# Kernel tuning notes

Hardware: AMD Instinct MI355X
Metric: run time of the kernel (lower is better)

The kernel has to match this reference:

```python
import jax, jax.numpy as jnp
import numpy as np

N = 100000   # batched tree nodes
WD = 300     # word_dim
TD = 50      # tag_dim
M = 168      # mem_dim


def setup_inputs() -> dict:
    key = jax.random.key(0)
    ks = jax.random.split(key, 17)
    rn = lambda k, shp: jax.random.normal(k, shp, dtype=jnp.float32)
    w = lambda k, shp: jax.random.normal(k, shp, dtype=jnp.float32) * 0.05
    return {
        "e": rn(ks[0], (N, WD)),
        "tag": rn(ks[1], (N, TD)),
        "tag_parent": rn(ks[2], (N, TD)),
        "h_prev": rn(ks[3], (N, M)),
        "c_prev": rn(ks[4], (N, M)),
        "k": rn(ks[5], (N, M)),
        "q": rn(ks[6], (N, M)),
        # Leaf cell: 4 gates (i, o, f_left, u), each with We/Wt/Wtp/Uh linears,
        # fused as stacked [in_dim, 4*M] matrices + one fused bias.
        "We_l": w(ks[7], (WD, 4 * M)),
        "Wt_l": w(ks[8], (TD, 4 * M)),
        "Wtp_l": w(ks[9], (TD, 4 * M)),
        "Uh_l": w(ks[10], (M, 4 * M)),
        "b_l": w(ks[11], (4 * M,)),
        # Node cell: 5 gates (i, o, f_left, f_down, u) with Wt/Wtp/Uh; the Uk
        # (child-sum k) linear is only applied to the first 4 gates (u omits it,
        # per the source).
        "Wt_n": w(ks[12], (TD, 5 * M)),
        "Wtp_n": w(ks[13], (TD, 5 * M)),
        "Uh_n": w(ks[14], (M, 5 * M)),
        "Uk_n": w(ks[15], (M, 4 * M)),
        "b_n": w(ks[16], (5 * M,)),
    }


def reference(e, tag, tag_parent, h_prev, c_prev, k, q,
              We_l, Wt_l, Wtp_l, Uh_l, b_l,
              Wt_n, Wtp_n, Uh_n, Uk_n, b_n):
    sig, tanh = jax.nn.sigmoid, jnp.tanh
    # ---- LeafModule ----
    pre = e @ We_l + tag @ Wt_l + tag_parent @ Wtp_l + h_prev @ Uh_l + b_l  # [N, 4M]
    i, o, fl, u = jnp.split(pre, 4, axis=-1)
    c1 = sig(i) * tanh(u) + sig(fl) * c_prev
    h1 = sig(o) * tanh(c1)
    # ---- NodeModule (consumes leaf state as h_prev / c_prev) ----
    pre5 = tag @ Wt_n + tag_parent @ Wtp_n + h1 @ Uh_n + b_n  # [N, 5M]
    pre4 = k @ Uk_n                                            # [N, 4M]
    i2, o2, fl2, fd2, u2 = jnp.split(pre5, 5, axis=-1)
    ki, ko, kfl, kfd = jnp.split(pre4, 4, axis=-1)
    i2, o2, fl2, fd2 = i2 + ki, o2 + ko, fl2 + kfl, fd2 + kfd
    c2 = sig(i2) * tanh(u2) + sig(fd2) * q + sig(fl2) * c1
    h2 = sig(o2) * tanh(c2)
    return jnp.concatenate([h2, c2], axis=-1)  # [N, 2M]
```

## Files before the change

### kernel.cpp

```cpp
#include <hip/hip_runtime.h>
#include <hip/hip_bf16.h>

#define NROWS 100000

typedef __attribute__((ext_vector_type(8))) short bf16x8;
typedef __attribute__((ext_vector_type(4))) float f32x4;
typedef float f32x4a8 __attribute__((ext_vector_type(4), aligned(8)));

__device__ __forceinline__ short f2b(float f) {
  __hip_bfloat16 h = __float2bfloat16(f);
  short s;
  __builtin_memcpy(&s, &h, sizeof(s));
  return s;
}

__device__ __forceinline__ float b2f(unsigned short u) {
  unsigned v = ((unsigned)u) << 16;
  float f;
  __builtin_memcpy(&f, &v, sizeof(f));
  return f;
}

__device__ __forceinline__ float sigf(float x) { return 1.f / (1.f + __expf(-x)); }
__device__ __forceinline__ float tanh_f(float x) { return 1.f - 2.f / (__expf(2.f * x) + 1.f); }

__device__ __forceinline__ void gload_lds16(const void* g, void* l) {
  __builtin_amdgcn_global_load_lds((const __attribute__((address_space(1))) unsigned int*)g,
                                   (__attribute__((address_space(3))) unsigned int*)l, 16, 0, 0);
}

__global__ void pack_weights(const float* __restrict__ We_l, const float* __restrict__ Wt_l,
                             const float* __restrict__ Wtp_l, const float* __restrict__ Uh_l,
                             const float* __restrict__ b_l,
                             const float* __restrict__ Wt_n, const float* __restrict__ Wtp_n,
                             const float* __restrict__ Uh_n, const float* __restrict__ Uk_n,
                             const float* __restrict__ b_n,
                             unsigned short* __restrict__ B1, unsigned short* __restrict__ B2) {
  const int NB1 = 18 * 3 * 16 * 512;
  const int NB2 = 14 * 3 * 24 * 512;
  int idx = blockIdx.x * blockDim.x + threadIdx.x;
  if (idx < NB1) {
    int b = idx & 7, lane = (idx >> 3) & 63, t = idx >> 9;
    int ct = t % 16, mb = (t / 16) % 3, kt = t / 48;
    int k = kt * 32 + ((lane >> 4) << 3) + b;
    int gate = ct >> 2, mtl = ct & 3;
    int m = mb * 64 + mtl * 16 + (lane & 15);
    float v = 0.f;
    if (m < 168) {
      int col = gate * 168 + m;
      if (k < 300)       v = We_l[k * 672 + col];
      else if (k < 350)  v = Wt_l[(k - 300) * 672 + col];
      else if (k < 400)  v = Wtp_l[(k - 350) * 672 + col];
      else if (k < 568)  v = Uh_l[(k - 400) * 672 + col];
      else if (k == 568) v = b_l[col];
    }
    B1[idx] = (unsigned short)f2b(v);
  } else if (idx < NB1 + NB2) {
    int j = idx - NB1;
    int b = j & 7, lane = (j >> 3) & 63, t = j >> 9;
    int ct = t % 24, mb = (t / 24) % 3, kt = t / 72;
    int k = kt * 32 + ((lane >> 4) << 3) + b;
    int gate = ct >> 2, mtl = ct & 3;
    int m = mb * 64 + mtl * 16 + (lane & 15);
    float v = 0.f;
    if (ct < 20 && m < 168) {
      int col = gate * 168 + m;
      if (k < 50)        v = Wt_n[k * 840 + col];
      else if (k < 100)  v = Wtp_n[(k - 50) * 840 + col];
      else if (k < 268)  v = (gate < 4) ? Uk_n[(k - 100) * 672 + gate * 168 + m] : 0.f;
      else if (k < 436)  v = Uh_n[(k - 268) * 840 + col];
      else if (k == 436) v = b_n[col];
    }
    B2[j] = (unsigned short)f2b(v);
  }
}

__device__ __forceinline__ float4 ld4a8(const float* __restrict__ p) {
  f32x4a8 v = *(const f32x4a8*)p;
  return make_float4(v[0], v[1], v[2], v[3]);
}

#define G1_NKT 18
#define G1_LOADS 2

__global__ __launch_bounds__(512, 4) void gemm1_kernel(
    const float* __restrict__ e, const float* __restrict__ tg, const float* __restrict__ tp,
    const float* __restrict__ hp, const float* __restrict__ cprev,
    const char* __restrict__ B1, unsigned short* __restrict__ c1buf,
    unsigned short* __restrict__ h1buf) {
  __shared__ char bb[2][16 * 1024];
  __shared__ char ab[2][4096];
  const int tid = threadIdx.x;
  const int wave = tid >> 6, ln = tid & 63;
  const int rw = wave >> 2, cw = wave & 3;
  const int rowblk = blockIdx.x / 3, mb = blockIdx.x % 3;
  const int rbase = rowblk * 64 + rw * 32;
  const int c = ln & 15, rg = ln >> 4;

  const int srowt = tid >> 3;
  const int sks = tid & 7;
  int srow = rowblk * 64 + srowt;
  if (srow >= NROWS) srow = NROWS - 1;
  const int sphys = srowt * 64 + ((((sks >> 1) ^ ((srowt >> 1) & 3)) << 4)) + ((sks & 1) << 3);

  auto loadA = [&](int kt) -> float4 {
    const int c4 = kt * 32 + sks * 4;
    if (c4 + 4 <= 300) return *(const float4*)(e + srow * 300 + c4);
    if (c4 >= 300 && c4 + 4 <= 348) return ld4a8(tg + srow * 50 + (c4 - 300));
    if (c4 == 348)
      return make_float4(tg[srow * 50 + 48], tg[srow * 50 + 49], tp[srow * 50 + 0], tp[srow * 50 + 1]);
    if (c4 >= 352 && c4 + 4 <= 400) return ld4a8(tp + srow * 50 + (c4 - 350));
    if (c4 >= 400 && c4 + 4 <= 568) return *(const float4*)(hp + srow * 168 + (c4 - 400));
    if (c4 == 568) return make_float4(1.f, 0.f, 0.f, 0.f);
    return make_float4(0.f, 0.f, 0.f, 0.f);
  };
  auto storeA = [&](int buf, float4 v) {
    ushort4 w;
    w.x = (unsigned short)f2b(v.x); w.y = (unsigned short)f2b(v.y);
    w.z = (unsigned short)f2b(v.z); w.w = (unsigned short)f2b(v.w);
    *(ushort4*)&ab[buf][sphys] = w;
  };

  f32x4 acc[2][4];
  const f32x4 z4 = {0.f, 0.f, 0.f, 0.f};
#pragma unroll
  for (int a = 0; a < 2; ++a)
#pragma unroll
    for (int t = 0; t < 4; ++t) acc[a][t] = z4;

  storeA(0, loadA(0));
  const char* Bbase = B1 + (size_t)mb * 16384;
#pragma unroll
  for (int j = 0; j < G1_LOADS; ++j)
    gload_lds16(Bbase + (j * 512 + tid) * 16, &bb[0][(j * 512 + (wave << 6)) * 16]);
  float4 av = loadA(1);
  __syncthreads();

  const int r0t = rw * 32 + c, r1t = rw * 32 + 16 + c;
  const int aoff0 = r0t * 64 + ((rg ^ ((r0t >> 1) & 3)) << 4);
  const int aoff1 = r1t * 64 + ((rg ^ ((r1t >> 1) & 3)) << 4);

#pragma unroll
  for (int kt = 0; kt < G1_NKT; ++kt) {
    const int cur = kt & 1, nxt = cur ^ 1;
    bf16x8 a0 = *(const bf16x8*)&ab[cur][aoff0];
    bf16x8 a1 = *(const bf16x8*)&ab[cur][aoff1];
    bf16x8 bfr[4];
#pragma unroll
    for (int g = 0; g < 4; ++g)
      bfr[g] = *(const bf16x8*)&bb[cur][((((g << 2) + cw) << 6) + ln) * 16];
    if (kt + 1 < G1_NKT) {
      storeA(nxt, av);
      if (kt + 2 < G1_NKT) av = loadA(kt + 2);
      const char* g = B1 + ((size_t)(kt + 1) * 3 + mb) * 16384;
#pragma unroll
      for (int j = 0; j < G1_LOADS; ++j)
        gload_lds16(g + (j * 512 + tid) * 16, &bb[nxt][(j * 512 + (wave << 6)) * 16]);
    }
#pragma unroll
    for (int g = 0; g < 4; ++g) {
      acc[0][g] = __builtin_amdgcn_mfma_f32_16x16x32_bf16(a0, bfr[g], acc[0][g], 0, 0, 0);
      acc[1][g] = __builtin_amdgcn_mfma_f32_16x16x32_bf16(a1, bfr[g], acc[1][g], 0, 0, 0);
    }
    __syncthreads();
  }

  const int m = mb * 64 + cw * 16 + c;
  if (m < 168) {
#pragma unroll
    for (int rt = 0; rt < 2; ++rt) {
#pragma unroll
      for (int reg = 0; reg < 4; ++reg) {
        const int row = rbase + rt * 16 + (rg << 2) + reg;
        if (row >= NROWS) continue;
        const float iv = acc[rt][0][reg];
        const float ov = acc[rt][1][reg];
        const float fv = acc[rt][2][reg];
        const float uv = acc[rt][3][reg];
        const int off = row * 168 + m;
        const float cp = cprev[off];
        const float c1 = sigf(iv) * tanh_f(uv) + sigf(fv) * cp;
        const float h1 = sigf(ov) * tanh_f(c1);
        c1buf[off] = (unsigned short)f2b(c1);
        h1buf[off] = (unsigned short)f2b(h1);
      }
    }
  }
}

#define G2_NKT 14
#define G2_LOADS 3

__global__ __launch_bounds__(512, 4) void gemm2_kernel(
    const float* __restrict__ tg, const float* __restrict__ tp, const float* __restrict__ kk,
    const float* __restrict__ q, const char* __restrict__ B2,
    const unsigned short* __restrict__ c1buf, const unsigned short* __restrict__ h1buf,
    float* __restrict__ out) {
  __shared__ char bb[2][24 * 1024];
  __shared__ char ab[2][4096];
  const int tid = threadIdx.x;
  const int wave = tid >> 6, ln = tid & 63;
  const int rw = wave >> 2, cw = wave & 3;
  const int rowblk = blockIdx.x / 3, mb = blockIdx.x % 3;
  const int rbase = rowblk * 64 + rw * 32;
  const int c = ln & 15, rg = ln >> 4;

  const int srowt = tid >> 3;
  const int sks = tid & 7;
  int srow = rowblk * 64 + srowt;
  if (srow >= NROWS) srow = NROWS - 1;
  const int sphys = srowt * 64 + ((((sks >> 1) ^ ((srowt >> 1) & 3)) << 4)) + ((sks & 1) << 3);

  auto loadA = [&](int kt) -> float4 {
    const int c4 = kt * 32 + sks * 4;
    if (c4 + 4 <= 48) return ld4a8(tg + srow * 50 + c4);
    if (c4 == 48)
      return make_float4(tg[srow * 50 + 48], tg[srow * 50 + 49], tp[srow * 50 + 0], tp[srow * 50 + 1]);
    if (c4 >= 52 && c4 + 4 <= 100) return ld4a8(tp + srow * 50 + (c4 - 50));
    if (c4 >= 100 && c4 + 4 <= 268) return *(const float4*)(kk + srow * 168 + (c4 - 100));
    if (c4 >= 268 && c4 + 4 <= 436) {
      ushort4 w = *(const ushort4*)(h1buf + srow * 168 + (c4 - 268));
      return make_float4(b2f(w.x), b2f(w.y), b2f(w.z), b2f(w.w));
    }
    if (c4 == 436) return make_float4(1.f, 0.f, 0.f, 0.f);
    return make_float4(0.f, 0.f, 0.f, 0.f);
  };
  auto storeA = [&](int buf, float4 v) {
    ushort4 w;
    w.x = (unsigned short)f2b(v.x); w.y = (unsigned short)f2b(v.y);
    w.z = (unsigned short)f2b(v.z); w.w = (unsigned short)f2b(v.w);
    *(ushort4*)&ab[buf][sphys] = w;
  };

  f32x4 acc[2][5];
  const f32x4 z4 = {0.f, 0.f, 0.f, 0.f};
#pragma unroll
  for (int a = 0; a < 2; ++a)
#pragma unroll
    for (int t = 0; t < 5; ++t) acc[a][t] = z4;

  storeA(0, loadA(0));
  const char* Bbase = B2 + (size_t)mb * 24576;
#pragma unroll
  for (int j = 0; j < G2_LOADS; ++j)
    gload_lds16(Bbase + (j * 512 + tid) * 16, &bb[0][(j * 512 + (wave << 6)) * 16]);
  float4 av = loadA(1);
  __syncthreads();

  const int r0t = rw * 32 + c, r1t = rw * 32 + 16 + c;
  const int aoff0 = r0t * 64 + ((rg ^ ((r0t >> 1) & 3)) << 4);
  const int aoff1 = r1t * 64 + ((rg ^ ((r1t >> 1) & 3)) << 4);

#pragma unroll
  for (int kt = 0; kt < G2_NKT; ++kt) {
    const int cur = kt & 1, nxt = cur ^ 1;
    bf16x8 a0 = *(const bf16x8*)&ab[cur][aoff0];
    bf16x8 a1 = *(const bf16x8*)&ab[cur][aoff1];
    bf16x8 bfr[5];
#pragma unroll
    for (int g = 0; g < 5; ++g)
      bfr[g] = *(const bf16x8*)&bb[cur][((((g << 2) + cw) << 6) + ln) * 16];
    if (kt + 1 < G2_NKT) {
      storeA(nxt, av);
      if (kt + 2 < G2_NKT) av = loadA(kt + 2);
      const char* g = B2 + ((size_t)(kt + 1) * 3 + mb) * 24576;
#pragma unroll
      for (int j = 0; j < G2_LOADS; ++j)
        gload_lds16(g + (j * 512 + tid) * 16, &bb[nxt][(j * 512 + (wave << 6)) * 16]);
    }
#pragma unroll
    for (int g = 0; g < 5; ++g) {
      acc[0][g] = __builtin_amdgcn_mfma_f32_16x16x32_bf16(a0, bfr[g], acc[0][g], 0, 0, 0);
      acc[1][g] = __builtin_amdgcn_mfma_f32_16x16x32_bf16(a1, bfr[g], acc[1][g], 0, 0, 0);
    }
    __syncthreads();
  }

  const int m = mb * 64 + cw * 16 + c;
  if (m < 168) {
#pragma unroll
    for (int rt = 0; rt < 2; ++rt) {
#pragma unroll
      for (int reg = 0; reg < 4; ++reg) {
        const int row = rbase + rt * 16 + (rg << 2) + reg;
        if (row >= NROWS) continue;
        const float i2 = acc[rt][0][reg];
        const float o2 = acc[rt][1][reg];
        const float fl2 = acc[rt][2][reg];
        const float fd2 = acc[rt][3][reg];
        const float u2 = acc[rt][4][reg];
        const int off = row * 168 + m;
        const float c1 = b2f(c1buf[off]);
        const float qv = q[off];
        const float c2 = sigf(i2) * tanh_f(u2) + sigf(fd2) * qv + sigf(fl2) * c1;
        const float h2 = sigf(o2) * tanh_f(c2);
        out[row * 336 + m] = h2;
        out[row * 336 + 168 + m] = c2;
      }
    }
  }
}

extern "C" void kernel_launch(void* const* d_in, const int* in_sizes, int n_in,
                              void* d_out, int out_size, void* d_ws, size_t ws_size,
                              hipStream_t stream) {
  const float* e     = (const float*)d_in[0];
  const float* tag   = (const float*)d_in[1];
  const float* tagp  = (const float*)d_in[2];
  const float* hprev = (const float*)d_in[3];
  const float* cprev = (const float*)d_in[4];
  const float* kk    = (const float*)d_in[5];
  const float* q     = (const float*)d_in[6];
  const float* We_l  = (const float*)d_in[7];
  const float* Wt_l  = (const float*)d_in[8];
  const float* Wtp_l = (const float*)d_in[9];
  const float* Uh_l  = (const float*)d_in[10];
  const float* b_l   = (const float*)d_in[11];
  const float* Wt_n  = (const float*)d_in[12];
  const float* Wtp_n = (const float*)d_in[13];
  const float* Uh_n  = (const float*)d_in[14];
  const float* Uk_n  = (const float*)d_in[15];
  const float* b_n   = (const float*)d_in[16];
  float* out = (float*)d_out;

  char* ws = (char*)d_ws;
  unsigned short* B1 = (unsigned short*)ws;
  unsigned short* B2 = (unsigned short*)(ws + (1 << 20));
  unsigned short* c1buf = (unsigned short*)(ws + (3 << 20));
  unsigned short* h1buf = (unsigned short*)(ws + (3 << 20) + 33600000);

  const int NB = 18 * 3 * 16 * 512 + 14 * 3 * 24 * 512;
  pack_weights<<<(NB + 255) / 256, 256, 0, stream>>>(We_l, Wt_l, Wtp_l, Uh_l, b_l,
                                                     Wt_n, Wtp_n, Uh_n, Uk_n, b_n, B1, B2);

  const int nblk = ((NROWS + 63) / 64) * 3;
  gemm1_kernel<<<nblk, 512, 0, stream>>>(e, tag, tagp, hprev, cprev,
                                         (const char*)B1, c1buf, h1buf);
  gemm2_kernel<<<nblk, 512, 0, stream>>>(tag, tagp, kk, q,
                                         (const char*)B2, c1buf, h1buf, out);
}
```

Before: 489.7 us.

## Replace LDS-staged GEMMs with per-wave register tiles loading operands directly

Both GEMM kernels drop shared-memory staging and barriers. Each wave now owns a 64-row (gemm1) or 48-row (gemm2) by 16-column tile covering all gates. A and B fragments are loaded straight from global memory into registers with double-buffered prefetch. The weight packing is reordered per column tile, and the node cell's K order puts h1 first so its bf16 data can be fed to MFMA without conversion. This removes LDS traffic and __syncthreads, but gives up cross-wave reuse of A and B through LDS, so global and L2 loads rise and register pressure grows.

```diff
diff --git a/kernel.cpp b/kernel.cpp
--- a/kernel.cpp
+++ b/kernel.cpp
@@ -2,6 +2,10 @@
 #include <hip/hip_bf16.h>
 
 #define NROWS 100000
+#define G1_NRB 1563
+#define G2_NRB 2084
+#define G1_NT (G1_NRB * 11)
+#define G2_NT (G2_NRB * 11)
 
 typedef __attribute__((ext_vector_type(8))) short bf16x8;
 typedef __attribute__((ext_vector_type(4))) float f32x4;
@@ -14,20 +18,35 @@
   return s;
 }
 
-__device__ __forceinline__ float b2f(unsigned short u) {
-  unsigned v = ((unsigned)u) << 16;
-  float f;
-  __builtin_memcpy(&f, &v, sizeof(f));
-  return f;
-}
-
 __device__ __forceinline__ float sigf(float x) { return 1.f / (1.f + __expf(-x)); }
 __device__ __forceinline__ float tanh_f(float x) { return 1.f - 2.f / (__expf(2.f * x) + 1.f); }
 
-__device__ __forceinline__ void gload_lds16(const void* g, void* l) {
-  __builtin_amdgcn_global_load_lds((const __attribute__((address_space(1))) unsigned int*)g,
-                                   (__attribute__((address_space(3))) unsigned int*)l, 16, 0, 0);
-}
+__device__ __forceinline__ float4 ld4a8(const float* __restrict__ p) {
+  f32x4a8 v = *(const f32x4a8*)p;
+  return make_float4(v[0], v[1], v[2], v[3]);
+}
+
+__device__ __forceinline__ float4 u2f4(uint4 u) {
+  float4 f;
+  __builtin_memcpy(&f, &u, 16);
+  return f;
+}
+
+__device__ __forceinline__ bf16x8 raw2bf8(float4 lo) {
+  bf16x8 r;
+  __builtin_memcpy(&r, &lo, 16);
+  return r;
+}
+
+__device__ __forceinline__ bf16x8 cvt2bf8(float4 lo, float4 hi) {
+  bf16x8 r;
+  r[0] = f2b(lo.x); r[1] = f2b(lo.y); r[2] = f2b(lo.z); r[3] = f2b(lo.w);
+  r[4] = f2b(hi.x); r[5] = f2b(hi.y); r[6] = f2b(hi.z); r[7] = f2b(hi.w);
+  return r;
+}
+
+#define NB1R (18 * 11 * 4 * 512)
+#define NB2R (14 * 11 * 5 * 512)
 
 __global__ void pack_weights(const float* __restrict__ We_l, const float* __restrict__ Wt_l,
                              const float* __restrict__ Wtp_l, const float* __restrict__ Uh_l,
@@ -35,16 +54,14 @@
                              const float* __restrict__ Wt_n, const float* __restrict__ Wtp_n,
                              const float* __restrict__ Uh_n, const float* __restrict__ Uk_n,
                              const float* __restrict__ b_n,
-                             unsigned short* __restrict__ B1, unsigned short* __restrict__ B2) {
-  const int NB1 = 18 * 3 * 16 * 512;
-  const int NB2 = 14 * 3 * 24 * 512;
+                             unsigned short* __restrict__ B1r, unsigned short* __restrict__ B2r) {
   int idx = blockIdx.x * blockDim.x + threadIdx.x;
-  if (idx < NB1) {
-    int b = idx & 7, lane = (idx >> 3) & 63, t = idx >> 9;
-    int ct = t % 16, mb = (t / 16) % 3, kt = t / 48;
+  if (idx < NB1R) {
+    int b = idx & 7, lane = (idx >> 3) & 63, fr = idx >> 9;
+    int gate = fr & 3, tmp = fr >> 2;
+    int mt = tmp % 11, kt = tmp / 11;
     int k = kt * 32 + ((lane >> 4) << 3) + b;
-    int gate = ct >> 2, mtl = ct & 3;
-    int m = mb * 64 + mtl * 16 + (lane & 15);
+    int m = mt * 16 + (lane & 15);
     float v = 0.f;
     if (m < 168) {
       int col = gate * 168 + m;
@@ -54,130 +71,122 @@
       else if (k < 568)  v = Uh_l[(k - 400) * 672 + col];
       else if (k == 568) v = b_l[col];
     }
-    B1[idx] = (unsigned short)f2b(v);
-  } else if (idx < NB1 + NB2) {
-    int j = idx - NB1;
-    int b = j & 7, lane = (j >> 3) & 63, t = j >> 9;
-    int ct = t % 24, mb = (t / 24) % 3, kt = t / 72;
+    B1r[idx] = (unsigned short)f2b(v);
+  } else if (idx < NB1R + NB2R) {
+    int j = idx - NB1R;
+    int b = j & 7, lane = (j >> 3) & 63, fr = j >> 9;
+    int gate = fr % 5, tmp = fr / 5;
+    int mt = tmp % 11, kt = tmp / 11;
     int k = kt * 32 + ((lane >> 4) << 3) + b;
-    int gate = ct >> 2, mtl = ct & 3;
-    int m = mb * 64 + mtl * 16 + (lane & 15);
+    int m = mt * 16 + (lane & 15);
     float v = 0.f;
-    if (ct < 20 && m < 168) {
+    if (m < 168) {
       int col = gate * 168 + m;
-      if (k < 50)        v = Wt_n[k * 840 + col];
-      else if (k < 100)  v = Wtp_n[(k - 50) * 840 + col];
-      else if (k < 268)  v = (gate < 4) ? Uk_n[(k - 100) * 672 + gate * 168 + m] : 0.f;
-      else if (k < 436)  v = Uh_n[(k - 268) * 840 + col];
+      if (k < 168)       v = Uh_n[k * 840 + col];
+      else if (k < 218)  v = Wt_n[(k - 168) * 840 + col];
+      else if (k < 268)  v = Wtp_n[(k - 218) * 840 + col];
+      else if (k < 436)  v = (gate < 4) ? Uk_n[(k - 268) * 672 + gate * 168 + m] : 0.f;
       else if (k == 436) v = b_n[col];
     }
-    B2[j] = (unsigned short)f2b(v);
-  }
-}
-
-__device__ __forceinline__ float4 ld4a8(const float* __restrict__ p) {
-  f32x4a8 v = *(const f32x4a8*)p;
-  return make_float4(v[0], v[1], v[2], v[3]);
-}
-
-#define G1_NKT 18
-#define G1_LOADS 2
-
-__global__ __launch_bounds__(512, 4) void gemm1_kernel(
+    B2r[j] = (unsigned short)f2b(v);
+  }
+}
+
+__global__ __launch_bounds__(256, 3) void gemm1_kernel(
     const float* __restrict__ e, const float* __restrict__ tg, const float* __restrict__ tp,
     const float* __restrict__ hp, const float* __restrict__ cprev,
-    const char* __restrict__ B1, unsigned short* __restrict__ c1buf,
+    const unsigned short* __restrict__ B1r, unsigned short* __restrict__ c1buf,
     unsigned short* __restrict__ h1buf) {
-  __shared__ char bb[2][16 * 1024];
-  __shared__ char ab[2][4096];
-  const int tid = threadIdx.x;
-  const int wave = tid >> 6, ln = tid & 63;
-  const int rw = wave >> 2, cw = wave & 3;
-  const int rowblk = blockIdx.x / 3, mb = blockIdx.x % 3;
-  const int rbase = rowblk * 64 + rw * 32;
+  const int tid = threadIdx.x, wave = tid >> 6, ln = tid & 63;
+  const int wid = blockIdx.x * 4 + wave;
+  if (wid >= G1_NT) return;
+  const int rb = wid / 11, mt = wid - rb * 11;
   const int c = ln & 15, rg = ln >> 4;
-
-  const int srowt = tid >> 3;
-  const int sks = tid & 7;
-  int srow = rowblk * 64 + srowt;
-  if (srow >= NROWS) srow = NROWS - 1;
-  const int sphys = srowt * 64 + ((((sks >> 1) ^ ((srowt >> 1) & 3)) << 4)) + ((sks & 1) << 3);
-
-  auto loadA = [&](int kt) -> float4 {
-    const int c4 = kt * 32 + sks * 4;
-    if (c4 + 4 <= 300) return *(const float4*)(e + srow * 300 + c4);
-    if (c4 >= 300 && c4 + 4 <= 348) return ld4a8(tg + srow * 50 + (c4 - 300));
-    if (c4 == 348)
-      return make_float4(tg[srow * 50 + 48], tg[srow * 50 + 49], tp[srow * 50 + 0], tp[srow * 50 + 1]);
-    if (c4 >= 352 && c4 + 4 <= 400) return ld4a8(tp + srow * 50 + (c4 - 350));
-    if (c4 >= 400 && c4 + 4 <= 568) return *(const float4*)(hp + srow * 168 + (c4 - 400));
-    if (c4 == 568) return make_float4(1.f, 0.f, 0.f, 0.f);
-    return make_float4(0.f, 0.f, 0.f, 0.f);
+  const int k0base = rg << 3;
+
+  int row[4];
+#pragma unroll
+  for (int rt = 0; rt < 4; ++rt) {
+    int r = rb * 64 + rt * 16 + c;
+    row[rt] = r < NROWS ? r : NROWS - 1;
+  }
+  const char* bptr = (const char*)B1r + (size_t)mt * 4096 + (size_t)ln * 16;
+
+  auto loadA = [&](int kt, int rt, float4& lo, float4& hi) {
+    const int k0 = kt * 32 + k0base;
+    const int r = row[rt];
+    if (k0 + 8 <= 300) {
+      const float* p = e + r * 300 + k0;
+      lo = *(const float4*)p; hi = *(const float4*)(p + 4);
+    } else if (k0 == 296) {
+      lo = *(const float4*)(e + r * 300 + 296);
+      hi = ld4a8(tg + r * 50);
+    } else if (k0 >= 304 && k0 + 8 <= 350) {
+      const float* p = tg + r * 50 + (k0 - 300);
+      lo = ld4a8(p); hi = ld4a8(p + 4);
+    } else if (k0 == 344) {
+      lo = ld4a8(tg + r * 50 + 44);
+      hi = make_float4(tg[r * 50 + 48], tg[r * 50 + 49], tp[r * 50 + 0], tp[r * 50 + 1]);
+    } else if (k0 >= 352 && k0 + 8 <= 400) {
+      const float* p = tp + r * 50 + (k0 - 350);
+      lo = ld4a8(p); hi = ld4a8(p + 4);
+    } else if (k0 >= 400 && k0 + 8 <= 568) {
+      const float* p = hp + r * 168 + (k0 - 400);
+      lo = *(const float4*)p; hi = *(const float4*)(p + 4);
+    } else {
+      lo = make_float4(1.f, 0.f, 0.f, 0.f);
+      hi = make_float4(0.f, 0.f, 0.f, 0.f);
+    }
   };
-  auto storeA = [&](int buf, float4 v) {
-    ushort4 w;
-    w.x = (unsigned short)f2b(v.x); w.y = (unsigned short)f2b(v.y);
-    w.z = (unsigned short)f2b(v.z); w.w = (unsigned short)f2b(v.w);
-    *(ushort4*)&ab[buf][sphys] = w;
+  auto loadB = [&](int kt, int g) -> bf16x8 {
+    return *(const bf16x8*)(bptr + (size_t)kt * 45056 + (size_t)g * 1024);
   };
 
-  f32x4 acc[2][4];
+  f32x4 acc[4][4];
   const f32x4 z4 = {0.f, 0.f, 0.f, 0.f};
 #pragma unroll
-  for (int a = 0; a < 2; ++a)
-#pragma unroll
-    for (int t = 0; t < 4; ++t) acc[a][t] = z4;
-
-  storeA(0, loadA(0));
-  const char* Bbase = B1 + (size_t)mb * 16384;
-#pragma unroll
-  for (int j = 0; j < G1_LOADS; ++j)
-    gload_lds16(Bbase + (j * 512 + tid) * 16, &bb[0][(j * 512 + (wave << 6)) * 16]);
-  float4 av = loadA(1);
-  __syncthreads();
-
-  const int r0t = rw * 32 + c, r1t = rw * 32 + 16 + c;
-  const int aoff0 = r0t * 64 + ((rg ^ ((r0t >> 1) & 3)) << 4);
-  const int aoff1 = r1t * 64 + ((rg ^ ((r1t >> 1) & 3)) << 4);
-
-#pragma unroll
-  for (int kt = 0; kt < G1_NKT; ++kt) {
-    const int cur = kt & 1, nxt = cur ^ 1;
-    bf16x8 a0 = *(const bf16x8*)&ab[cur][aoff0];
-    bf16x8 a1 = *(const bf16x8*)&ab[cur][aoff1];
-    bf16x8 bfr[4];
-#pragma unroll
-    for (int g = 0; g < 4; ++g)
-      bfr[g] = *(const bf16x8*)&bb[cur][((((g << 2) + cw) << 6) + ln) * 16];
-    if (kt + 1 < G1_NKT) {
-      storeA(nxt, av);
-      if (kt + 2 < G1_NKT) av = loadA(kt + 2);
-      const char* g = B1 + ((size_t)(kt + 1) * 3 + mb) * 16384;
-#pragma unroll
-      for (int j = 0; j < G1_LOADS; ++j)
-        gload_lds16(g + (j * 512 + tid) * 16, &bb[nxt][(j * 512 + (wave << 6)) * 16]);
-    }
-#pragma unroll
-    for (int g = 0; g < 4; ++g) {
-      acc[0][g] = __builtin_amdgcn_mfma_f32_16x16x32_bf16(a0, bfr[g], acc[0][g], 0, 0, 0);
-      acc[1][g] = __builtin_amdgcn_mfma_f32_16x16x32_bf16(a1, bfr[g], acc[1][g], 0, 0, 0);
-    }
-    __syncthreads();
-  }
-
-  const int m = mb * 64 + cw * 16 + c;
+  for (int rt = 0; rt < 4; ++rt)
+#pragma unroll
+    for (int g = 0; g < 4; ++g) acc[rt][g] = z4;
+
+  float4 alo[4], ahi[4];
+  bf16x8 Bb[2][4];
+#pragma unroll
+  for (int rt = 0; rt < 4; ++rt) loadA(0, rt, alo[rt], ahi[rt]);
+#pragma unroll
+  for (int g = 0; g < 4; ++g) Bb[0][g] = loadB(0, g);
+
+#pragma unroll
+  for (int kt = 0; kt < 18; ++kt) {
+    bf16x8 af[4];
+#pragma unroll
+    for (int rt = 0; rt < 4; ++rt) af[rt] = cvt2bf8(alo[rt], ahi[rt]);
+    if (kt + 1 < 18) {
+#pragma unroll
+      for (int rt = 0; rt < 4; ++rt) loadA(kt + 1, rt, alo[rt], ahi[rt]);
+#pragma unroll
+      for (int g = 0; g < 4; ++g) Bb[(kt + 1) & 1][g] = loadB(kt + 1, g);
+    }
+#pragma unroll
+    for (int rt = 0; rt < 4; ++rt)
+#pragma unroll
+      for (int g = 0; g < 4; ++g)
+        acc[rt][g] = __builtin_amdgcn_mfma_f32_16x16x32_bf16(af[rt], Bb[kt & 1][g], acc[rt][g], 0, 0, 0);
+  }
+
+  const int m = mt * 16 + c;
   if (m < 168) {
 #pragma unroll
-    for (int rt = 0; rt < 2; ++rt) {
+    for (int rt = 0; rt < 4; ++rt) {
 #pragma unroll
       for (int reg = 0; reg < 4; ++reg) {
-        const int row = rbase + rt * 16 + (rg << 2) + reg;
-        if (row >= NROWS) continue;
+        const int r = rb * 64 + rt * 16 + (rg << 2) + reg;
+        if (r >= NROWS) continue;
         const float iv = acc[rt][0][reg];
         const float ov = acc[rt][1][reg];
         const float fv = acc[rt][2][reg];
         const float uv = acc[rt][3][reg];
-        const int off = row * 168 + m;
+        const int off = r * 168 + m;
         const float cp = cprev[off];
         const float c1 = sigf(iv) * tanh_f(uv) + sigf(fv) * cp;
         const float h1 = sigf(ov) * tanh_f(c1);
@@ -188,114 +197,115 @@
   }
 }
 
-#define G2_NKT 14
-#define G2_LOADS 3
-
-__global__ __launch_bounds__(512, 4) void gemm2_kernel(
+__global__ __launch_bounds__(256, 3) void gemm2_kernel(
     const float* __restrict__ tg, const float* __restrict__ tp, const float* __restrict__ kk,
-    const float* __restrict__ q, const char* __restrict__ B2,
+    const float* __restrict__ q, const unsigned short* __restrict__ B2r,
     const unsigned short* __restrict__ c1buf, const unsigned short* __restrict__ h1buf,
     float* __restrict__ out) {
-  __shared__ char bb[2][24 * 1024];
-  __shared__ char ab[2][4096];
-  const int tid = threadIdx.x;
-  const int wave = tid >> 6, ln = tid & 63;
-  const int rw = wave >> 2, cw = wave & 3;
-  const int rowblk = blockIdx.x / 3, mb = blockIdx.x % 3;
-  const int rbase = rowblk * 64 + rw * 32;
+  const int tid = threadIdx.x, wave = tid >> 6, ln = tid & 63;
+  const int wid = blockIdx.x * 4 + wave;
+  if (wid >= G2_NT) return;
+  const int rb = wid / 11, mt = wid - rb * 11;
   const int c = ln & 15, rg = ln >> 4;
-
-  const int srowt = tid >> 3;
-  const int sks = tid & 7;
-  int srow = rowblk * 64 + srowt;
-  if (srow >= NROWS) srow = NROWS - 1;
-  const int sphys = srowt * 64 + ((((sks >> 1) ^ ((srowt >> 1) & 3)) << 4)) + ((sks & 1) << 3);
-
-  auto loadA = [&](int kt) -> float4 {
-    const int c4 = kt * 32 + sks * 4;
-    if (c4 + 4 <= 48) return ld4a8(tg + srow * 50 + c4);
-    if (c4 == 48)
-      return make_float4(tg[srow * 50 + 48], tg[srow * 50 + 49], tp[srow * 50 + 0], tp[srow * 50 + 1]);
-    if (c4 >= 52 && c4 + 4 <= 100) return ld4a8(tp + srow * 50 + (c4 - 50));
-    if (c4 >= 100 && c4 + 4 <= 268) return *(const float4*)(kk + srow * 168 + (c4 - 100));
-    if (c4 >= 268 && c4 + 4 <= 436) {
-      ushort4 w = *(const ushort4*)(h1buf + srow * 168 + (c4 - 268));
-      return make_float4(b2f(w.x), b2f(w.y), b2f(w.z), b2f(w.w));
-    }
-    if (c4 == 436) return make_float4(1.f, 0.f, 0.f, 0.f);
-    return make_float4(0.f, 0.f, 0.f, 0.f);
+  const int k0base = rg << 3;
+
+  int row[3];
+#pragma unroll
+  for (int rt = 0; rt < 3; ++rt) {
+    int r = rb * 48 + rt * 16 + c;
+    row[rt] = r < NROWS ? r : NROWS - 1;
+  }
+  const char* bptr = (const char*)B2r + (size_t)mt * 5120 + (size_t)ln * 16;
+
+  auto loadA = [&](int kt, int rt, float4& lo, float4& hi) {
+    const int k0 = kt * 32 + k0base;
+    const int r = row[rt];
+    if (k0 + 8 <= 168) {
+      uint4 u = *(const uint4*)(h1buf + r * 168 + k0);
+      lo = u2f4(u);
+      hi = make_float4(0.f, 0.f, 0.f, 0.f);
+    } else if (k0 >= 168 && k0 + 8 <= 216) {
+      const float* p = tg + r * 50 + (k0 - 168);
+      lo = ld4a8(p); hi = ld4a8(p + 4);
+    } else if (k0 == 216) {
+      lo = make_float4(tg[r * 50 + 48], tg[r * 50 + 49], tp[r * 50 + 0], tp[r * 50 + 1]);
+      hi = ld4a8(tp + r * 50 + 2);
+    } else if (k0 >= 224 && k0 + 8 <= 264) {
+      const float* p = tp + r * 50 + (k0 - 218);
+      lo = ld4a8(p); hi = ld4a8(p + 4);
+    } else if (k0 == 264) {
+      lo = ld4a8(tp + r * 50 + 46);
+      hi = *(const float4*)(kk + r * 168);
+    } else if (k0 >= 272 && k0 + 8 <= 436) {
+      const float* p = kk + r * 168 + (k0 - 268);
+      lo = *(const float4*)p; hi = *(const float4*)(p + 4);
+    } else if (k0 == 432) {
+      lo = *(const float4*)(kk + r * 168 + 164);
+      hi = make_float4(1.f, 0.f, 0.f, 0.f);
+    } else {
+      lo = make_float4(0.f, 0.f, 0.f, 0.f);
+      hi = make_float4(0.f, 0.f, 0.f, 0.f);
+    }
   };
-  auto storeA = [&](int buf, float4 v) {
-    ushort4 w;
-    w.x = (unsigned short)f2b(v.x); w.y = (unsigned short)f2b(v.y);
-    w.z = (unsigned short)f2b(v.z); w.w = (unsigned short)f2b(v.w);
-    *(ushort4*)&ab[buf][sphys] = w;
+  auto loadB = [&](int kt, int g) -> bf16x8 {
+    return *(const bf16x8*)(bptr + (size_t)kt * 56320 + (size_t)g * 1024);
   };
 
-  f32x4 acc[2][5];
+  f32x4 acc[3][5];
   const f32x4 z4 = {0.f, 0.f, 0.f, 0.f};
 #pragma unroll
-  for (int a = 0; a < 2; ++a)
-#pragma unroll
-    for (int t = 0; t < 5; ++t) acc[a][t] = z4;
-
-  storeA(0, loadA(0));
-  const char* Bbase = B2 + (size_t)mb * 24576;
-#pragma unroll
-  for (int j = 0; j < G2_LOADS; ++j)
-    gload_lds16(Bbase + (j * 512 + tid) * 16, &bb[0][(j * 512 + (wave << 6)) * 16]);
-  float4 av = loadA(1);
-  __syncthreads();
-
-  const int r0t = rw * 32 + c, r1t = rw * 32 + 16 + c;
-  const int aoff0 = r0t * 64 + ((rg ^ ((r0t >> 1) & 3)) << 4);
-  const int aoff1 = r1t * 64 + ((rg ^ ((r1t >> 1) & 3)) << 4);
-
-#pragma unroll
-  for (int kt = 0; kt < G2_NKT; ++kt) {
-    const int cur = kt & 1, nxt = cur ^ 1;
-    bf16x8 a0 = *(const bf16x8*)&ab[cur][aoff0];
-    bf16x8 a1 = *(const bf16x8*)&ab[cur][aoff1];
-    bf16x8 bfr[5];
-#pragma unroll
-    for (int g = 0; g < 5; ++g)
-      bfr[g] = *(const bf16x8*)&bb[cur][((((g << 2) + cw) << 6) + ln) * 16];
-    if (kt + 1 < G2_NKT) {
-      storeA(nxt, av);
-      if (kt + 2 < G2_NKT) av = loadA(kt + 2);
-      const char* g = B2 + ((size_t)(kt + 1) * 3 + mb) * 24576;
-#pragma unroll
-      for (int j = 0; j < G2_LOADS; ++j)
-        gload_lds16(g + (j * 512 + tid) * 16, &bb[nxt][(j * 512 + (wave << 6)) * 16]);
-    }
-#pragma unroll
-    for (int g = 0; g < 5; ++g) {
-      acc[0][g] = __builtin_amdgcn_mfma_f32_16x16x32_bf16(a0, bfr[g], acc[0][g], 0, 0, 0);
-      acc[1][g] = __builtin_amdgcn_mfma_f32_16x16x32_bf16(a1, bfr[g], acc[1][g], 0, 0, 0);
-    }
-    __syncthreads();
-  }
-
-  const int m = mb * 64 + cw * 16 + c;
+  for (int rt = 0; rt < 3; ++rt)
+#pragma unroll
+    for (int g = 0; g < 5; ++g) acc[rt][g] = z4;
+
+  float4 alo[3], ahi[3];
+  bf16x8 Bb[2][5];
+#pragma unroll
+  for (int rt = 0; rt < 3; ++rt) loadA(0, rt, alo[rt], ahi[rt]);
+#pragma unroll
+  for (int g = 0; g < 5; ++g) Bb[0][g] = loadB(0, g);
+
+#pragma unroll
+  for (int kt = 0; kt < 14; ++kt) {
+    const int k0 = kt * 32 + k0base;
+    const bool ish1 = (k0 + 8 <= 168);
+    bf16x8 af[3];
+#pragma unroll
+    for (int rt = 0; rt < 3; ++rt)
+      af[rt] = ish1 ? raw2bf8(alo[rt]) : cvt2bf8(alo[rt], ahi[rt]);
+    if (kt + 1 < 14) {
+#pragma unroll
+      for (int rt = 0; rt < 3; ++rt) loadA(kt + 1, rt, alo[rt], ahi[rt]);
+#pragma unroll
+      for (int g = 0; g < 5; ++g) Bb[(kt + 1) & 1][g] = loadB(kt + 1, g);
+    }
+#pragma unroll
+    for (int rt = 0; rt < 3; ++rt)
+#pragma unroll
+      for (int g = 0; g < 5; ++g)
+        acc[rt][g] = __builtin_amdgcn_mfma_f32_16x16x32_bf16(af[rt], Bb[kt & 1][g], acc[rt][g], 0, 0, 0);
+  }
+
+  const int m = mt * 16 + c;
   if (m < 168) {
 #pragma unroll
-    for (int rt = 0; rt < 2; ++rt) {
+    for (int rt = 0; rt < 3; ++rt) {
 #pragma unroll
       for (int reg = 0; reg < 4; ++reg) {
-        const int row = rbase + rt * 16 + (rg << 2) + reg;
-        if (row >= NROWS) continue;
+        const int r = rb * 48 + rt * 16 + (rg << 2) + reg;
+        if (r >= NROWS) continue;
         const float i2 = acc[rt][0][reg];
         const float o2 = acc[rt][1][reg];
         const float fl2 = acc[rt][2][reg];
         const float fd2 = acc[rt][3][reg];
         const float u2 = acc[rt][4][reg];
-        const int off = row * 168 + m;
-        const float c1 = b2f(c1buf[off]);
+        const int off = r * 168 + m;
+        const float c1 = __bfloat162float(*(const __hip_bfloat16*)&c1buf[off]);
         const float qv = q[off];
         const float c2 = sigf(i2) * tanh_f(u2) + sigf(fd2) * qv + sigf(fl2) * c1;
         const float h2 = sigf(o2) * tanh_f(c2);
-        out[row * 336 + m] = h2;
-        out[row * 336 + 168 + m] = c2;
+        out[r * 336 + m] = h2;
+        out[r * 336 + 168 + m] = c2;
       }
     }
   }
@@ -324,18 +334,17 @@
   float* out = (float*)d_out;
 
   char* ws = (char*)d_ws;
-  unsigned short* B1 = (unsigned short*)ws;
-  unsigned short* B2 = (unsigned short*)(ws + (1 << 20));
-  unsigned short* c1buf = (unsigned short*)(ws + (3 << 20));
-  unsigned short* h1buf = (unsigned short*)(ws + (3 << 20) + 33600000);
-
-  const int NB = 18 * 3 * 16 * 512 + 14 * 3 * 24 * 512;
+  unsigned short* B1r = (unsigned short*)ws;
+  unsigned short* B2r = (unsigned short*)(ws + (1 << 20));
+  unsigned short* c1buf = (unsigned short*)(ws + (2 << 20));
+  unsigned short* h1buf = (unsigned short*)(ws + (2 << 20) + 33600000);
+
+  const int NB = NB1R + NB2R;
   pack_weights<<<(NB + 255) / 256, 256, 0, stream>>>(We_l, Wt_l, Wtp_l, Uh_l, b_l,
-                                                     Wt_n, Wtp_n, Uh_n, Uk_n, b_n, B1, B2);
-
-  const int nblk = ((NROWS + 63) / 64) * 3;
-  gemm1_kernel<<<nblk, 512, 0, stream>>>(e, tag, tagp, hprev, cprev,
-                                         (const char*)B1, c1buf, h1buf);
-  gemm2_kernel<<<nblk, 512, 0, stream>>>(tag, tagp, kk, q,
-                                         (const char*)B2, c1buf, h1buf, out);
-}
+                                                     Wt_n, Wtp_n, Uh_n, Uk_n, b_n, B1r, B2r);
+
+  gemm1_kernel<<<(G1_NT + 3) / 4, 256, 0, stream>>>(e, tag, tagp, hprev, cprev,
+                                                    B1r, c1buf, h1buf);
+  gemm2_kernel<<<(G2_NT + 3) / 4, 256, 0, stream>>>(tag, tagp, kk, q,
+                                                    B2r, c1buf, h1buf, out);
+}
```

New measurement: 679.0 us. 38.7% more time.
